# Performance work log

Measured on AMD Instinct MI355X. Metric: run time of the kernel, lower is better.

The kernel has to match this reference:

```python
import math
import jax, jax.numpy as jnp
import numpy as np

B, S, D, H = 4, 2048, 1024, 16
DK = D // H


def setup_inputs() -> dict:
    key = jax.random.key(0)
    ks = jax.random.split(key, 12)
    s = 1.0 / math.sqrt(D)
    return {
        "query": jax.random.normal(ks[0], (B, S, D), dtype=jnp.float32),
        "key": jax.random.normal(ks[1], (B, S, D), dtype=jnp.float32),
        "value": jax.random.normal(ks[2], (B, S, D), dtype=jnp.float32),
        "mask": jax.random.randint(ks[3], (B, 1, S), 0, 2, dtype=jnp.int32),
        "Wq": jax.random.normal(ks[4], (D, D), dtype=jnp.float32) * s,
        "bq": jnp.zeros((D,), dtype=jnp.float32),
        "Wk": jax.random.normal(ks[5], (D, D), dtype=jnp.float32) * s,
        "bk": jnp.zeros((D,), dtype=jnp.float32),
        "Wv": jax.random.normal(ks[6], (D, D), dtype=jnp.float32) * s,
        "bv": jnp.zeros((D,), dtype=jnp.float32),
        "Wo": jax.random.normal(ks[7], (D, D), dtype=jnp.float32) * s,
        "bo": jnp.zeros((D,), dtype=jnp.float32),
    }


def reference(query, key, value, mask, Wq, bq, Wk, bk, Wv, bv, Wo, bo):
    # Projections (torch Linear: x @ W.T + b), split into heads: [B,H,S,DK]
    def proj(x, W, b):
        return (x @ W.T + b).reshape(B, -1, H, DK).transpose(0, 2, 1, 3)

    q = proj(query, Wq, bq)
    k = proj(key, Wk, bk)
    v = proj(value, Wv, bv)

    scale = 1.0 / math.sqrt(DK)
    scores = jnp.einsum("bhqd,bhkd->bhqk", q, k) * scale  # [B,H,S,S]
    m = mask[:, None, :, :]  # [B,1,1,S] broadcasts over heads and query dim
    scores = jnp.where(m == 0, jnp.float32(-1e9), scores)
    p_attn = jax.nn.softmax(scores, axis=-1)
    # dropout is identity in eval mode (deterministic reference)
    x = jnp.einsum("bhqk,bhkd->bhqd", p_attn, v)  # [B,H,S,DK]
    x = x.transpose(0, 2, 1, 3).reshape(B, -1, D)  # [B,S,D]
    return x @ Wo.T + bo
```

## Files before the change

kernel.cpp:

```cpp
#include <hip/hip_runtime.h>
#include <hip/hip_bf16.h>
#include <stdint.h>

typedef __bf16 bf16;
typedef __bf16 bf16x8 __attribute__((ext_vector_type(8)));
typedef float f32x4 __attribute__((ext_vector_type(4)));
typedef float f32x16 __attribute__((ext_vector_type(16)));
typedef unsigned short u16;
typedef unsigned int u32;
typedef unsigned int u32x4 __attribute__((ext_vector_type(4)));

__device__ static inline u16 f2bf_bits(float f) {
    __bf16 b = (__bf16)f;
    return __builtin_bit_cast(u16, b);
}

__device__ static inline u32 packbf(float a, float b) {
    return (u32)f2bf_bits(a) | ((u32)f2bf_bits(b) << 16);
}

typedef __attribute__((address_space(1))) const u32 gl_u32;
typedef __attribute__((address_space(3))) u32 lo_u32;

__device__ static inline void gload_lds16(const void* gp, void* lp) {
    __builtin_amdgcn_global_load_lds((gl_u32*)gp, (lo_u32*)lp, 16, 0, 0);
}

__device__ static inline int pi64(int r) {
    return (r & ~12) | ((r & 4) << 1) | ((r & 8) >> 1);
}

__global__ void cvt_all(const float* __restrict__ q, const float* __restrict__ k,
                        const float* __restrict__ v, const float* __restrict__ wq,
                        const float* __restrict__ wk, const float* __restrict__ wv,
                        const float* __restrict__ wo, u16* __restrict__ oq,
                        u16* __restrict__ ok, u16* __restrict__ ov,
                        u16* __restrict__ owq, u16* __restrict__ owk,
                        u16* __restrict__ owv, u16* __restrict__ owo) {
    const int i = blockIdx.x * blockDim.x + threadIdx.x;
    const float* src;
    u16* dst;
    int j;
    if (i < 3 * 2097152) {
        const int t = i >> 21;
        j = i & ((1 << 21) - 1);
        src = t == 0 ? q : t == 1 ? k : v;
        dst = t == 0 ? oq : t == 1 ? ok : ov;
    } else {
        const int w2 = i - 3 * 2097152;
        const int t = w2 >> 18;
        j = w2 & ((1 << 18) - 1);
        src = t == 0 ? wq : t == 1 ? wk : t == 2 ? wv : wo;
        dst = t == 0 ? owq : t == 1 ? owk : t == 2 ? owv : owo;
    }
    float4 f = ((const float4*)src)[j];
    ushort4 o;
    o.x = f2bf_bits(f.x);
    o.y = f2bf_bits(f.y);
    o.z = f2bf_bits(f.z);
    o.w = f2bf_bits(f.w);
    ((ushort4*)dst)[j] = o;
}

template <int MODE>
__device__ __forceinline__ void gemm_body(unsigned char* As, unsigned char* Bs,
                                          const bf16* __restrict__ A,
                                          const bf16* __restrict__ W,
                                          const float* __restrict__ bias,
                                          float scale, void* __restrict__ Out,
                                          const int* __restrict__ Msk,
                                          int bm, int bn) {
    constexpr int K = 1024;
    const int tid = threadIdx.x;
    const int lane = tid & 63, w = tid >> 6;
    const int l15 = lane & 15, l4 = lane >> 4;
    const int wr = w >> 1, wc = w & 1;
    const int m0 = bm * 128, n0 = bn * 128;

    f32x4 acc[4][4] = {};

    int aoff[4], boff[4];
#pragma unroll
    for (int i = 0; i < 4; ++i) {
        aoff[i] = (wr * 64 + i * 16 + l15) * 64 + l4 * 16;
        boff[i] = (wc * 64 + i * 16 + l15) * 64 + l4 * 16;
    }

    const int c0 = tid, c1 = 256 + tid;
    const int ar0 = m0 + (c0 >> 2), ar1 = m0 + (c1 >> 2);
    const int br0 = n0 + (c0 >> 2), br1 = n0 + (c1 >> 2);
    const int sl0 = (c0 & 3) * 8, sl1 = (c1 & 3) * 8;

    for (int k0 = 0; k0 < K; k0 += 32) {
        __syncthreads();
        gload_lds16(A + (size_t)ar0 * K + k0 + sl0, As + w * 1024);
        gload_lds16(A + (size_t)ar1 * K + k0 + sl1, As + 4096 + w * 1024);
        gload_lds16(W + (size_t)br0 * K + k0 + sl0, Bs + w * 1024);
        gload_lds16(W + (size_t)br1 * K + k0 + sl1, Bs + 4096 + w * 1024);
        __syncthreads();
        bf16x8 af[4], bfr[4];
#pragma unroll
        for (int i = 0; i < 4; ++i) af[i] = *(const bf16x8*)(As + aoff[i]);
#pragma unroll
        for (int i = 0; i < 4; ++i) bfr[i] = *(const bf16x8*)(Bs + boff[i]);
#pragma unroll
        for (int mi = 0; mi < 4; ++mi)
#pragma unroll
            for (int ni = 0; ni < 4; ++ni)
                acc[mi][ni] = __builtin_amdgcn_mfma_f32_16x16x32_bf16(af[mi], bfr[ni], acc[mi][ni], 0, 0, 0);
    }

#pragma unroll
    for (int mi = 0; mi < 4; ++mi) {
        const int mb = m0 + wr * 64 + mi * 16 + l4 * 4;
        int4 mv = {1, 1, 1, 1};
        if (MODE == 1) {
            const int bb = mb >> 11, s = mb & 2047;
            mv = *(const int4*)(Msk + bb * 2048 + s);
        }
#pragma unroll
        for (int ni = 0; ni < 4; ++ni) {
            const int n = n0 + wc * 64 + ni * 16 + l15;
            const float bv = bias[n];
            if (MODE == 0) {
                const int hh = n >> 6, dk = n & 63;
#pragma unroll
                for (int r = 0; r < 4; ++r) {
                    const int m = mb + r;
                    const int bb = m >> 11, s = m & 2047;
                    ((u16*)Out)[(((size_t)bb * 16 + hh) * 2048 + s) * 64 + dk] =
                        f2bf_bits((acc[mi][ni][r] + bv) * scale);
                }
            } else if (MODE == 1) {
                const int hh = n >> 6, dk = n & 63;
                const int bb = mb >> 11, s = mb & 2047;
                ushort4 pk;
                pk.x = f2bf_bits(mv.x ? (acc[mi][ni][0] + bv) : 0.0f);
                pk.y = f2bf_bits(mv.y ? (acc[mi][ni][1] + bv) : 0.0f);
                pk.z = f2bf_bits(mv.z ? (acc[mi][ni][2] + bv) : 0.0f);
                pk.w = f2bf_bits(mv.w ? (acc[mi][ni][3] + bv) : 0.0f);
                *(ushort4*)((u16*)Out + (((size_t)bb * 16 + hh) * 64 + dk) * 2048 + s) = pk;
            } else {
#pragma unroll
                for (int r = 0; r < 4; ++r) {
                    const int m = mb + r;
                    ((float*)Out)[(size_t)m * 1024 + n] = (acc[mi][ni][r] + bv) * scale;
                }
            }
        }
    }
}

__global__ __launch_bounds__(256) void gemm_qkv(const bf16* __restrict__ xq,
                                                const bf16* __restrict__ xk,
                                                const bf16* __restrict__ xv,
                                                const bf16* __restrict__ wq,
                                                const bf16* __restrict__ wk,
                                                const bf16* __restrict__ wv,
                                                const float* __restrict__ bq,
                                                const float* __restrict__ bk,
                                                const float* __restrict__ bv,
                                                const int* __restrict__ msk,
                                                u16* __restrict__ Qb,
                                                u16* __restrict__ Kb,
                                                u16* __restrict__ Vtb) {
    __shared__ unsigned char As[8192];
    __shared__ unsigned char Bs[8192];
    const int lb = blockIdx.x;
    const int wg = (lb & 7) * 192 + (lb >> 3);
    const int grp = wg >> 9, inner = wg & 511;
    const int bm = inner >> 3, bn = inner & 7;
    const float qscale = 0.125f * 1.44269504088896340736f;
    if (grp == 2) {
        gemm_body<1>(As, Bs, xv, wv, bv, 1.0f, (void*)Vtb, msk, bm, bn);
    } else if (grp == 1) {
        gemm_body<0>(As, Bs, xk, wk, bk, 1.0f, (void*)Kb, nullptr, bm, bn);
    } else {
        gemm_body<0>(As, Bs, xq, wq, bq, qscale, (void*)Qb, nullptr, bm, bn);
    }
}

__global__ __launch_bounds__(256) void gemm_out(const bf16* __restrict__ A,
                                                const bf16* __restrict__ W,
                                                const float* __restrict__ bias,
                                                float* __restrict__ Out) {
    __shared__ unsigned char As[8192];
    __shared__ unsigned char Bs[8192];
    const int lb = blockIdx.x;
    const int wg = (lb & 7) * 64 + (lb >> 3);
    gemm_body<2>(As, Bs, A, W, bias, 1.0f, (void*)Out, nullptr, wg >> 3, wg & 7);
}

__global__ __launch_bounds__(256, 4) void attn_kernel(const bf16* __restrict__ Q,
                                                      const bf16* __restrict__ Kg,
                                                      const bf16* __restrict__ Vt,
                                                      const int* __restrict__ msk,
                                                      u16* __restrict__ Xa) {
    constexpr int S = 2048;
    constexpr int NT = S / 64;
    __shared__ unsigned char Ks[2][8192];
    __shared__ unsigned char Vs[2][8192];
    __shared__ u16 maskf[2048];

    const int tid = threadIdx.x;
    const int lane = tid & 63;
    const int w = tid >> 6;
    const int l31 = lane & 31;
    const int hi = lane >> 5;

    const int lb = blockIdx.x;
    const int wg = (lb & 7) * 128 + (lb >> 3);
    const int bh = wg >> 4;
    const int q0 = (wg & 15) * 128;
    const int b = bh >> 4, h = bh & 15;

    const bf16* Kbh = Kg + (size_t)bh * S * 64;
    const bf16* Vbh = Vt + (size_t)bh * 64 * S;
    const int* mb = msk + b * S;

    {
        const int mi0 = tid * 8;
        const int4 a = *(const int4*)(mb + mi0);
        const int4 c = *(const int4*)(mb + mi0 + 4);
        ushort4 h0, h1;
        h0.x = a.x ? 0x3F80 : 0; h0.y = a.y ? 0x3F80 : 0;
        h0.z = a.z ? 0x3F80 : 0; h0.w = a.w ? 0x3F80 : 0;
        h1.x = c.x ? 0x3F80 : 0; h1.y = c.y ? 0x3F80 : 0;
        h1.z = c.z ? 0x3F80 : 0; h1.w = c.w ? 0x3F80 : 0;
        *(ushort4*)(&maskf[mi0]) = h0;
        *(ushort4*)(&maskf[mi0 + 4]) = h1;
    }

    const bf16* Qrow = Q + ((size_t)bh * S + q0 + w * 32 + l31) * 64 + hi * 8;
    bf16x8 qf[4];
#pragma unroll
    for (int d = 0; d < 4; ++d) qf[d] = *(const bf16x8*)(Qrow + d * 16);

    const int row0 = tid >> 4;
    const int lc = (tid & 15) ^ row0;
    const int sub = lc >> 3, wcol = lc & 7;
    const bf16* Ksrc = Kbh + (size_t)(pi64(row0) + 32 * sub) * 64 + wcol * 8;
    const bf16* Vsrc = Vbh + (size_t)(row0 + 32 * sub) * S + wcol * 8;

    gload_lds16(Ksrc, &Ks[0][w * 1024]);
    gload_lds16(Ksrc + 1024, &Ks[0][4096 + w * 1024]);
    gload_lds16(Vsrc, &Vs[0][w * 1024]);
    gload_lds16(Vsrc + 16 * S, &Vs[0][4096 + w * 1024]);

    f32x16 ot0 = {}, ot1 = {};
    f32x16 lacc = {};

    const int krow = l31 * 256;
    const int key = (l31 & 15) << 4;

    __syncthreads();

#pragma unroll 2
    for (int kt = 0; kt < NT; ++kt) {
        const int cur = kt & 1;
        if (kt + 1 < NT) {
            gload_lds16(Ksrc + (kt + 1) * 4096, &Ks[cur ^ 1][w * 1024]);
            gload_lds16(Ksrc + (kt + 1) * 4096 + 1024, &Ks[cur ^ 1][4096 + w * 1024]);
            gload_lds16(Vsrc + (kt + 1) * 64, &Vs[cur ^ 1][w * 1024]);
            gload_lds16(Vsrc + (kt + 1) * 64 + 16 * S, &Vs[cur ^ 1][4096 + w * 1024]);
        }

        const unsigned char* Kc = Ks[cur];
        f32x16 st0 = {}, st1 = {};
        __builtin_amdgcn_s_setprio(1);
#pragma unroll
        for (int d = 0; d < 4; ++d) {
            const int base = (((2 * d + hi) << 4) ^ key);
            bf16x8 kf0 = *(const bf16x8*)(Kc + krow + base);
            bf16x8 kf1 = *(const bf16x8*)(Kc + krow + (base ^ 128));
            st0 = __builtin_amdgcn_mfma_f32_32x32x16_bf16(kf0, qf[d], st0, 0, 0, 0);
            st1 = __builtin_amdgcn_mfma_f32_32x32x16_bf16(kf1, qf[d], st1, 0, 0, 0);
        }
        __builtin_amdgcn_s_setprio(0);

#pragma unroll
        for (int r = 0; r < 16; ++r) {
            st0[r] = __builtin_amdgcn_exp2f(st0[r] - 16.0f);
            st1[r] = __builtin_amdgcn_exp2f(st1[r] - 16.0f);
        }

        bf16x8 pb[4];
#pragma unroll
        for (int s = 0; s < 4; ++s) {
            const int off = (s & 1) * 8;
            u32x4 wd;
            if (s < 2) {
                wd.x = packbf(st0[off + 0], st0[off + 1]);
                wd.y = packbf(st0[off + 2], st0[off + 3]);
                wd.z = packbf(st0[off + 4], st0[off + 5]);
                wd.w = packbf(st0[off + 6], st0[off + 7]);
            } else {
                wd.x = packbf(st1[off + 0], st1[off + 1]);
                wd.y = packbf(st1[off + 2], st1[off + 3]);
                wd.z = packbf(st1[off + 4], st1[off + 5]);
                wd.w = packbf(st1[off + 6], st1[off + 7]);
            }
            pb[s] = __builtin_bit_cast(bf16x8, wd);
        }

        const unsigned char* Vc = Vs[cur];
        const u16* mrow_p = &maskf[kt * 64 + hi * 8];
        __builtin_amdgcn_s_setprio(1);
#pragma unroll
        for (int s = 0; s < 4; ++s) {
            const int base = (((2 * s + hi) << 4) ^ key);
            bf16x8 vf0 = *(const bf16x8*)(Vc + krow + base);
            bf16x8 vf1 = *(const bf16x8*)(Vc + krow + (base ^ 128));
            bf16x8 mf = *(const bf16x8*)(mrow_p + s * 16);
            ot0 = __builtin_amdgcn_mfma_f32_32x32x16_bf16(vf0, pb[s], ot0, 0, 0, 0);
            ot1 = __builtin_amdgcn_mfma_f32_32x32x16_bf16(vf1, pb[s], ot1, 0, 0, 0);
            lacc = __builtin_amdgcn_mfma_f32_32x32x16_bf16(mf, pb[s], lacc, 0, 0, 0);
        }
        __builtin_amdgcn_s_setprio(0);

        __syncthreads();
    }

    const float inv = 1.0f / lacc[0];
    const int qg = q0 + w * 32 + l31;
    u16* orow = Xa + ((size_t)(b * 2048 + qg)) * 1024 + h * 64 + hi * 4;
#pragma unroll
    for (int rg = 0; rg < 4; ++rg) {
        ushort4 o0, o1;
        o0.x = f2bf_bits(ot0[rg * 4 + 0] * inv);
        o0.y = f2bf_bits(ot0[rg * 4 + 1] * inv);
        o0.z = f2bf_bits(ot0[rg * 4 + 2] * inv);
        o0.w = f2bf_bits(ot0[rg * 4 + 3] * inv);
        o1.x = f2bf_bits(ot1[rg * 4 + 0] * inv);
        o1.y = f2bf_bits(ot1[rg * 4 + 1] * inv);
        o1.z = f2bf_bits(ot1[rg * 4 + 2] * inv);
        o1.w = f2bf_bits(ot1[rg * 4 + 3] * inv);
        *(ushort4*)(orow + rg * 8) = o0;
        *(ushort4*)(orow + 32 + rg * 8) = o1;
    }
}

extern "C" void kernel_launch(void* const* d_in, const int* in_sizes, int n_in,
                              void* d_out, int out_size, void* d_ws, size_t ws_size,
                              hipStream_t stream) {
    (void)in_sizes; (void)n_in; (void)out_size; (void)ws_size;
    const float* q_in = (const float*)d_in[0];
    const float* k_in = (const float*)d_in[1];
    const float* v_in = (const float*)d_in[2];
    const int* msk    = (const int*)d_in[3];
    const float* Wq = (const float*)d_in[4];
    const float* bq = (const float*)d_in[5];
    const float* Wk = (const float*)d_in[6];
    const float* bk = (const float*)d_in[7];
    const float* Wv = (const float*)d_in[8];
    const float* bv = (const float*)d_in[9];
    const float* Wo = (const float*)d_in[10];
    const float* bo = (const float*)d_in[11];

    char* ws = (char*)d_ws;
    const size_t MB = 1024ull * 1024ull;
    u16* xq  = (u16*)(ws + 0 * MB);
    u16* xk  = (u16*)(ws + 16 * MB);
    u16* xv  = (u16*)(ws + 32 * MB);
    u16* wqb = (u16*)(ws + 48 * MB);
    u16* wkb = (u16*)(ws + 50 * MB);
    u16* wvb = (u16*)(ws + 52 * MB);
    u16* wob = (u16*)(ws + 54 * MB);
    u16* Qb  = (u16*)(ws + 56 * MB);
    u16* Kb  = (u16*)(ws + 72 * MB);
    u16* Vtb = (u16*)(ws + 88 * MB);
    u16* Xa  = (u16*)(ws + 0 * MB);

    cvt_all<<<dim3(7340032 / 256), dim3(256), 0, stream>>>(q_in, k_in, v_in, Wq, Wk, Wv, Wo,
                                                           xq, xk, xv, wqb, wkb, wvb, wob);

    gemm_qkv<<<dim3(1536), dim3(256), 0, stream>>>((const bf16*)xq, (const bf16*)xk, (const bf16*)xv,
                                                   (const bf16*)wqb, (const bf16*)wkb, (const bf16*)wvb,
                                                   bq, bk, bv, msk, Qb, Kb, Vtb);

    attn_kernel<<<dim3(1024), dim3(256), 0, stream>>>((const bf16*)Qb, (const bf16*)Kb,
                                                      (const bf16*)Vtb, msk, Xa);

    gemm_out<<<dim3(512), dim3(256), 0, stream>>>((const bf16*)Xa, (const bf16*)wob, bo, (float*)d_out);
}
```

Measured before the change: 220.8 us.

## Software-pipeline attention loop: overlap QK^T of next tile with PV of previous

Restructures the attention inner loop into a prologue, steady state and epilogue. Each iteration computes QK^T and exp for tile kt while running the PV and row-sum MFMAs on the P values kept from tile kt-1, and loads V one tile later than K. The intent is to let the exp/pack VALU work overlap with matrix-core work from the other stage, removing the serial QK^T -> softmax -> PV dependency inside one iteration. In exchange, pb stays live across iterations, which raises register pressure, and the code is longer.

```diff
diff --git a/kernel.cpp b/kernel.cpp
--- a/kernel.cpp
+++ b/kernel.cpp
@@ -242,30 +242,24 @@
     const bf16* Ksrc = Kbh + (size_t)(pi64(row0) + 32 * sub) * 64 + wcol * 8;
     const bf16* Vsrc = Vbh + (size_t)(row0 + 32 * sub) * S + wcol * 8;
 
+    f32x16 ot0 = {}, ot1 = {};
+    f32x16 lacc = {};
+    bf16x8 pb[4];
+
+    const int krow = l31 * 256;
+    const int key = (l31 & 15) << 4;
+
     gload_lds16(Ksrc, &Ks[0][w * 1024]);
     gload_lds16(Ksrc + 1024, &Ks[0][4096 + w * 1024]);
-    gload_lds16(Vsrc, &Vs[0][w * 1024]);
-    gload_lds16(Vsrc + 16 * S, &Vs[0][4096 + w * 1024]);
-
-    f32x16 ot0 = {}, ot1 = {};
-    f32x16 lacc = {};
-
-    const int krow = l31 * 256;
-    const int key = (l31 & 15) << 4;
-
     __syncthreads();
 
-#pragma unroll 2
-    for (int kt = 0; kt < NT; ++kt) {
-        const int cur = kt & 1;
-        if (kt + 1 < NT) {
-            gload_lds16(Ksrc + (kt + 1) * 4096, &Ks[cur ^ 1][w * 1024]);
-            gload_lds16(Ksrc + (kt + 1) * 4096 + 1024, &Ks[cur ^ 1][4096 + w * 1024]);
-            gload_lds16(Vsrc + (kt + 1) * 64, &Vs[cur ^ 1][w * 1024]);
-            gload_lds16(Vsrc + (kt + 1) * 64 + 16 * S, &Vs[cur ^ 1][4096 + w * 1024]);
-        }
-
-        const unsigned char* Kc = Ks[cur];
+    {
+        gload_lds16(Ksrc + 4096, &Ks[1][w * 1024]);
+        gload_lds16(Ksrc + 4096 + 1024, &Ks[1][4096 + w * 1024]);
+        gload_lds16(Vsrc, &Vs[0][w * 1024]);
+        gload_lds16(Vsrc + 16 * S, &Vs[0][4096 + w * 1024]);
+
+        const unsigned char* Kc = Ks[0];
         f32x16 st0 = {}, st1 = {};
         __builtin_amdgcn_s_setprio(1);
 #pragma unroll
@@ -277,14 +271,11 @@
             st1 = __builtin_amdgcn_mfma_f32_32x32x16_bf16(kf1, qf[d], st1, 0, 0, 0);
         }
         __builtin_amdgcn_s_setprio(0);
-
 #pragma unroll
         for (int r = 0; r < 16; ++r) {
             st0[r] = __builtin_amdgcn_exp2f(st0[r] - 16.0f);
             st1[r] = __builtin_amdgcn_exp2f(st1[r] - 16.0f);
         }
-
-        bf16x8 pb[4];
 #pragma unroll
         for (int s = 0; s < 4; ++s) {
             const int off = (s & 1) * 8;
@@ -302,10 +293,33 @@
             }
             pb[s] = __builtin_bit_cast(bf16x8, wd);
         }
-
-        const unsigned char* Vc = Vs[cur];
-        const u16* mrow_p = &maskf[kt * 64 + hi * 8];
+        __syncthreads();
+    }
+
+#pragma unroll 2
+    for (int kt = 1; kt < NT; ++kt) {
+        const int cur = kt & 1, prv = cur ^ 1;
+        if (kt + 1 < NT) {
+            gload_lds16(Ksrc + (kt + 1) * 4096, &Ks[prv][w * 1024]);
+            gload_lds16(Ksrc + (kt + 1) * 4096 + 1024, &Ks[prv][4096 + w * 1024]);
+        }
+        gload_lds16(Vsrc + kt * 64, &Vs[cur][w * 1024]);
+        gload_lds16(Vsrc + kt * 64 + 16 * S, &Vs[cur][4096 + w * 1024]);
+
+        const unsigned char* Kc = Ks[cur];
+        f32x16 st0 = {}, st1 = {};
         __builtin_amdgcn_s_setprio(1);
+#pragma unroll
+        for (int d = 0; d < 4; ++d) {
+            const int base = (((2 * d + hi) << 4) ^ key);
+            bf16x8 kf0 = *(const bf16x8*)(Kc + krow + base);
+            bf16x8 kf1 = *(const bf16x8*)(Kc + krow + (base ^ 128));
+            st0 = __builtin_amdgcn_mfma_f32_32x32x16_bf16(kf0, qf[d], st0, 0, 0, 0);
+            st1 = __builtin_amdgcn_mfma_f32_32x32x16_bf16(kf1, qf[d], st1, 0, 0, 0);
+        }
+
+        const unsigned char* Vc = Vs[prv];
+        const u16* mrow_p = &maskf[(kt - 1) * 64 + hi * 8];
 #pragma unroll
         for (int s = 0; s < 4; ++s) {
             const int base = (((2 * s + hi) << 4) ^ key);
@@ -318,7 +332,47 @@
         }
         __builtin_amdgcn_s_setprio(0);
 
+#pragma unroll
+        for (int r = 0; r < 16; ++r) {
+            st0[r] = __builtin_amdgcn_exp2f(st0[r] - 16.0f);
+            st1[r] = __builtin_amdgcn_exp2f(st1[r] - 16.0f);
+        }
+#pragma unroll
+        for (int s = 0; s < 4; ++s) {
+            const int off = (s & 1) * 8;
+            u32x4 wd;
+            if (s < 2) {
+                wd.x = packbf(st0[off + 0], st0[off + 1]);
+                wd.y = packbf(st0[off + 2], st0[off + 3]);
+                wd.z = packbf(st0[off + 4], st0[off + 5]);
+                wd.w = packbf(st0[off + 6], st0[off + 7]);
+            } else {
+                wd.x = packbf(st1[off + 0], st1[off + 1]);
+                wd.y = packbf(st1[off + 2], st1[off + 3]);
+                wd.z = packbf(st1[off + 4], st1[off + 5]);
+                wd.w = packbf(st1[off + 6], st1[off + 7]);
+            }
+            pb[s] = __builtin_bit_cast(bf16x8, wd);
+        }
+
         __syncthreads();
+    }
+
+    {
+        const unsigned char* Vc = Vs[(NT - 1) & 1];
+        const u16* mrow_p = &maskf[(NT - 1) * 64 + hi * 8];
+        __builtin_amdgcn_s_setprio(1);
+#pragma unroll
+        for (int s = 0; s < 4; ++s) {
+            const int base = (((2 * s + hi) << 4) ^ key);
+            bf16x8 vf0 = *(const bf16x8*)(Vc + krow + base);
+            bf16x8 vf1 = *(const bf16x8*)(Vc + krow + (base ^ 128));
+            bf16x8 mf = *(const bf16x8*)(mrow_p + s * 16);
+            ot0 = __builtin_amdgcn_mfma_f32_32x32x16_bf16(vf0, pb[s], ot0, 0, 0, 0);
+            ot1 = __builtin_amdgcn_mfma_f32_32x32x16_bf16(vf1, pb[s], ot1, 0, 0, 0);
+            lacc = __builtin_amdgcn_mfma_f32_32x32x16_bf16(mf, pb[s], lacc, 0, 0, 0);
+        }
+        __builtin_amdgcn_s_setprio(0);
     }
 
     const float inv = 1.0f / lacc[0];
```

Measured after the change: 663.2 us. 3x slower.
